# Kernel tuning notes

Hardware: AMD Instinct MI355X
Metric: run time of the kernel (lower is better)

Reference implementation:

```python
import jax, jax.numpy as jnp
import numpy as np

K = 20          # knn neighbors (includes self, as in DGL KNNGraph)
EPS = 1e-5      # BatchNorm eps
SLOPE = 0.2     # leaky relu slope


def knn_idx(h, k):
    # h: [B,N,D]; k smallest pairwise squared distances (self included)
    d2 = jnp.sum(h * h, axis=-1)                                # [B,N]
    dist = d2[:, :, None] + d2[:, None, :] - 2.0 * jnp.einsum('bnd,bmd->bnm', h, h)
    _, idx = jax.lax.top_k(-dist, k)                            # [B,N,k] neighbor indices
    return idx


def edge_conv(h, idx, Wt, bt, Wp, bp, gamma, beta):
    # DGL EdgeConv with batch_norm=True (training-mode batch stats):
    # edges: src=neighbor j, dst=point i;  m_ij = theta(x_i - x_j) + phi(x_j)
    xj = jax.vmap(lambda hb, ib: hb[ib])(h, idx)                # [B,N,k,D] gathered neighbors
    m = (jnp.einsum('bnkd,do->bnko', h[:, :, None, :] - xj, Wt) + bt
         + jnp.einsum('bnkd,do->bnko', xj, Wp) + bp)            # [B,N,k,O]
    mu = jnp.mean(m, axis=(0, 1, 2))
    var = jnp.var(m, axis=(0, 1, 2))
    m = (m - mu) * jax.lax.rsqrt(var + EPS) * gamma + beta
    return jnp.max(m, axis=2)                                   # max aggregate over neighbors


def setup_inputs() -> dict:
    key = jax.random.key(0)
    ks = jax.random.split(key, 20)
    s = 0.05
    d_in, d0, d1, d_feat, d_out = 3, 64, 256, 512, 256
    return {
        'x':   jax.random.normal(ks[0], (4, 4096, d_in), jnp.float32),
        'Wt0': jax.random.normal(ks[1], (d_in, d0), jnp.float32) * s,
        'bt0': jnp.zeros((d0,), jnp.float32),
        'Wp0': jax.random.normal(ks[2], (d_in, d0), jnp.float32) * s,
        'bp0': jnp.zeros((d0,), jnp.float32),
        'g0':  jnp.ones((d0,), jnp.float32),
        'be0': jnp.zeros((d0,), jnp.float32),
        'Wt1': jax.random.normal(ks[3], (d0, d1), jnp.float32) * s,
        'bt1': jnp.zeros((d1,), jnp.float32),
        'Wp1': jax.random.normal(ks[4], (d0, d1), jnp.float32) * s,
        'bp1': jnp.zeros((d1,), jnp.float32),
        'g1':  jnp.ones((d1,), jnp.float32),
        'be1': jnp.zeros((d1,), jnp.float32),
        'Wg':  jax.random.normal(ks[5], (d1, 1), jnp.float32) * s,
        'bg':  jnp.zeros((1,), jnp.float32),
        'Wf':  jax.random.normal(ks[6], (d1, d_feat), jnp.float32) * s,
        'bf':  jnp.zeros((d_feat,), jnp.float32),
        'Wl':  jax.random.normal(ks[7], (d_feat, d_out), jnp.float32) * s,
        'bl':  jnp.zeros((d_out,), jnp.float32),
    }


def reference(x, Wt0, bt0, Wp0, bp0, g0, be0,
              Wt1, bt1, Wp1, bp1, g1, be1,
              Wg, bg, Wf, bf, Wl, bl):
    # layer 0: knn on raw points, EdgeConv 3->64, leaky relu
    h = x
    idx = knn_idx(h, K)
    h = jax.nn.leaky_relu(edge_conv(h, idx, Wt0, bt0, Wp0, bp0, g0, be0), SLOPE)
    # layer 1: knn on 64-d features, EdgeConv 64->256, leaky relu
    idx = knn_idx(h, K)
    h = jax.nn.leaky_relu(edge_conv(h, idx, Wt1, bt1, Wp1, bp1, g1, be1), SLOPE)
    # global attention pooling (softmax over nodes within each cloud)
    gate = jax.nn.relu(h @ Wg + bg)                 # [B,N,1]
    feat = jax.nn.relu(h @ Wf + bf)                 # [B,N,512]
    alpha = jax.nn.softmax(gate, axis=1)
    pooled = jnp.sum(alpha * feat, axis=1)          # [B,512]
    return pooled @ Wl + bl                         # [B,256]
```

## Files before the change

kernel.cpp:

```cpp
#include <hip/hip_runtime.h>
#include <hip/hip_bf16.h>
#include <math.h>

static constexpr int NBATCH = 4;
static constexpr int NPTS   = 4096;
static constexpr int BN     = NBATCH * NPTS;
static constexpr int KNN    = 20;
static constexpr float BN_EPS = 1e-5f;
static constexpr float SLOPE  = 0.2f;
static constexpr int DF = 512, DOUT = 256;

#define FINF __builtin_huge_valf()

typedef short bf16x8 __attribute__((ext_vector_type(8)));
typedef float f32x4  __attribute__((ext_vector_type(4)));

static constexpr size_t OFF_H0     = 0;
static constexpr size_t OFF_IDX0   = 4194304;
static constexpr size_t OFF_IDX1   = 5505024;
static constexpr size_t OFF_D2     = 6815744;
static constexpr size_t OFF_GATE   = 6881280;
static constexpr size_t OFF_ALPHA  = 6946816;
static constexpr size_t OFF_SS0    = 7012352;
static constexpr size_t OFF_SS1    = 7012864;
static constexpr size_t OFF_STATS0 = 7014912;
static constexpr size_t OFF_STATS1 = 7015424;
static constexpr size_t OFF_POOLED = 7017472;
static constexpr size_t ZERO_OFF   = OFF_STATS0;
static constexpr size_t ZERO_BYTES = 7025664 - 7014912;
static constexpr size_t OFF_P1     = 7025664;
static constexpr size_t OFF_PDU    = OFF_P1;
static constexpr size_t OFF_WQK    = 23802880;
static constexpr size_t OFF_WFK    = 23933952;
static constexpr size_t OFF_Q1     = 27997184;
static constexpr size_t OFF_U0     = OFF_Q1;
static constexpr size_t OFF_V0     = OFF_Q1 + 1048576;
static constexpr size_t OFF_P0     = OFF_Q1;
static constexpr size_t OFF_Q0     = OFF_Q1 + 2097152;
static constexpr size_t OFF_H1     = 44774400;
static constexpr size_t OFF_AB     = 61551616;

__device__ inline unsigned short f2bf_rne(float x) {
  unsigned int u = __float_as_uint(x);
  unsigned int lsb = (u >> 16) & 1u;
  u += 0x7fffu + lsb;
  return (unsigned short)(u >> 16);
}
__device__ inline float bf2f(unsigned short s) {
  return __uint_as_float((unsigned int)s << 16);
}
__device__ inline unsigned umn(unsigned a, unsigned b) { return a < b ? a : b; }
__device__ inline unsigned umed3(unsigned v, unsigned lo, unsigned hi) {
  unsigned d;
  asm("v_med3_u32 %0, %1, %2, %3" : "=v"(d) : "v"(v), "v"(lo), "v"(hi));
  return d;
}

__global__ __launch_bounds__(256) void d2x_kernel(const float* __restrict__ x,
                                                  float* __restrict__ d2) {
  int n = blockIdx.x * 256 + threadIdx.x;
  const float* r = x + (size_t)n * 3;
  d2[n] = r[0] * r[0] + r[1] * r[1] + r[2] * r[2];
}

__global__ __launch_bounds__(256) void usplit0_kernel(
    const float* __restrict__ x, unsigned short* __restrict__ U0,
    unsigned short* __restrict__ V0) {
  int n = blockIdx.x * 256 + threadIdx.x;
  float v0 = x[(size_t)n * 3], v1 = x[(size_t)n * 3 + 1], v2 = x[(size_t)n * 3 + 2];
  unsigned short A0 = f2bf_rne(v0), A1 = f2bf_rne(v1), A2 = f2bf_rne(v2);
  unsigned short B0 = f2bf_rne(v0 - bf2f(A0));
  unsigned short B1 = f2bf_rne(v1 - bf2f(A1));
  unsigned short B2 = f2bf_rne(v2 - bf2f(A2));
  ushort4 z = make_ushort4(0, 0, 0, 0);
  unsigned short* up = U0 + ((size_t)n << 5);
  ((ushort4*)up)[0] = make_ushort4(A0, A1, A2, B0);
  ((ushort4*)up)[1] = make_ushort4(B1, B2, A0, A1);
  ((ushort4*)up)[2] = make_ushort4(A2, B0, B1, B2);
  ((ushort4*)up)[3] = z; ((ushort4*)up)[4] = z; ((ushort4*)up)[5] = z;
  ((ushort4*)up)[6] = z; ((ushort4*)up)[7] = z;
  unsigned short* vp = V0 + ((size_t)n << 5);
  ((ushort4*)vp)[0] = make_ushort4(A0, A1, A2, A0);
  ((ushort4*)vp)[1] = make_ushort4(A1, A2, B0, B1);
  ((ushort4*)vp)[2] = make_ushort4(B2, B0, B1, B2);
  ((ushort4*)vp)[3] = z; ((ushort4*)vp)[4] = z; ((ushort4*)vp)[5] = z;
  ((ushort4*)vp)[6] = z; ((ushort4*)vp)[7] = z;
}

template<int KW, int CST, int S>
__global__ __launch_bounds__(256, 4) void knn_mfsel_kernel(
    const unsigned short* __restrict__ cab,
    const unsigned short* __restrict__ qab,
    const float* __restrict__ d2,
    unsigned* __restrict__ pdu) {
  constexpr int CS = NPTS / S, NCH = CS / 32;
  __shared__ __align__(16) unsigned short cbuf[2][32 * CST];
  __shared__ __align__(16) float cd2b[2][32];

  int bid = blockIdx.x;
  int s   = bid & (S - 1);
  int qb  = bid / S;
  int b   = qb >> 6;
  int qloc = (qb & 63) * 64;
  int wv = threadIdx.x >> 6, lane = threadIdx.x & 63;
  int l15 = lane & 15, lg = lane >> 4;
  int qg = b * NPTS + qloc + wv * 16 + l15;

  bf16x8 af[KW / 32];
#pragma unroll
  for (int kk = 0; kk < KW / 32; ++kk)
    af[kk] = *(const bf16x8*)(qab + (size_t)qg * KW + kk * 32 + lg * 8);
  float d2q = d2[qg];

  unsigned bd[KNN];
#pragma unroll
  for (int k = 0; k < KNN; ++k) bd[k] = 0xFFFFFFFFu;

  int scand = threadIdx.x >> 3, sseg = threadIdx.x & 7;
  const unsigned short* sbase = cab + ((size_t)(b * NPTS + s * CS)) * KW;
  const float* d2base = d2 + b * NPTS + s * CS;

  bf16x8 r0, r1;
  ushort4 r2;
  float rd2 = 0.f;

  if constexpr (KW == 128) {
    const unsigned short* src = sbase + (size_t)scand * KW + sseg * 16;
    r0 = *(const bf16x8*)src;
    r1 = *(const bf16x8*)(src + 8);
    *(bf16x8*)&cbuf[0][scand * CST + sseg * 16]     = r0;
    *(bf16x8*)&cbuf[0][scand * CST + sseg * 16 + 8] = r1;
  } else {
    r2 = *(const ushort4*)(sbase + (size_t)scand * KW + sseg * 4);
    *(ushort4*)&cbuf[0][scand * CST + sseg * 4] = r2;
  }
  if (threadIdx.x < 32) cd2b[0][threadIdx.x] = d2base[threadIdx.x];
  __syncthreads();

#pragma unroll 1
  for (int ch = 0; ch < NCH; ++ch) {
    int cur = ch & 1;
    if (ch < NCH - 1) {
      if constexpr (KW == 128) {
        const unsigned short* src = sbase + (size_t)(32 * (ch + 1) + scand) * KW + sseg * 16;
        r0 = *(const bf16x8*)src;
        r1 = *(const bf16x8*)(src + 8);
      } else {
        r2 = *(const ushort4*)(sbase + (size_t)(32 * (ch + 1) + scand) * KW + sseg * 4);
      }
      if (threadIdx.x < 32) rd2 = d2base[32 * (ch + 1) + threadIdx.x];
    }

    f32x4 acc0 = (f32x4){0.f, 0.f, 0.f, 0.f};
    f32x4 acc1 = (f32x4){0.f, 0.f, 0.f, 0.f};
    if constexpr (KW == 128) {
#pragma unroll
      for (int j = 0; j < 4; ++j) {
        int koff = j * 32 + lg * 8;
        bf16x8 a0 = *(const bf16x8*)&cbuf[cur][l15 * CST + koff];
        bf16x8 a1 = *(const bf16x8*)&cbuf[cur][(16 + l15) * CST + koff];
        acc0 = __builtin_amdgcn_mfma_f32_16x16x32_bf16(a0, af[j], acc0, 0, 0, 0);
        acc0 = __builtin_amdgcn_mfma_f32_16x16x32_bf16(a0, af[(j + 2) & 3], acc0, 0, 0, 0);
        acc1 = __builtin_amdgcn_mfma_f32_16x16x32_bf16(a1, af[j], acc1, 0, 0, 0);
        acc1 = __builtin_amdgcn_mfma_f32_16x16x32_bf16(a1, af[(j + 2) & 3], acc1, 0, 0, 0);
      }
    } else {
      bf16x8 a0 = *(const bf16x8*)&cbuf[cur][l15 * CST + lg * 8];
      bf16x8 a1 = *(const bf16x8*)&cbuf[cur][(16 + l15) * CST + lg * 8];
      acc0 = __builtin_amdgcn_mfma_f32_16x16x32_bf16(a0, af[0], acc0, 0, 0, 0);
      acc1 = __builtin_amdgcn_mfma_f32_16x16x32_bf16(a1, af[0], acc1, 0, 0, 0);
    }

    int cb = s * CS + ch * 32;
#pragma unroll
    for (int t = 0; t < 2; ++t) {
      f32x4 cd4 = *(const f32x4*)&cd2b[cur][t * 16 + lg * 4];
      f32x4 ac = t ? acc1 : acc0;
#pragma unroll
      for (int r = 0; r < 4; ++r) {
        float dist = fmaxf(fmaf(-2.f, ac[r], d2q + cd4[r]), 0.f);
        unsigned key = (__float_as_uint(dist) & 0xFFFFF000u)
                     | (unsigned)(cb + t * 16 + lg * 4 + r);
#pragma unroll
        for (int t_ = KNN - 1; t_ >= 1; --t_) bd[t_] = umed3(key, bd[t_ - 1], bd[t_]);
        bd[0] = umn(bd[0], key);
      }
    }

    if (ch < NCH - 1) {
      if constexpr (KW == 128) {
        *(bf16x8*)&cbuf[cur ^ 1][scand * CST + sseg * 16]     = r0;
        *(bf16x8*)&cbuf[cur ^ 1][scand * CST + sseg * 16 + 8] = r1;
      } else {
        *(ushort4*)&cbuf[cur ^ 1][scand * CST + sseg * 4] = r2;
      }
      if (threadIdx.x < 32) cd2b[cur ^ 1][threadIdx.x] = rd2;
    }
    __syncthreads();
  }

#pragma unroll 1
  for (int li = 1; li < 4; ++li) {
#pragma unroll 1
    for (int k = 0; k < KNN; ++k) {
      unsigned v = __shfl(bd[k], l15 + li * 16, 64);
      if (lg == 0 && v < bd[KNN - 1]) {
#pragma unroll
        for (int t_ = KNN - 1; t_ >= 1; --t_) bd[t_] = umed3(v, bd[t_ - 1], bd[t_]);
        bd[0] = umn(bd[0], v);
      }
    }
  }
  if (lg == 0) {
    unsigned* dst = pdu + ((size_t)(b * NPTS + qloc + wv * 16 + l15) * S + s) * KNN;
#pragma unroll
    for (int k = 0; k < KNN; ++k) dst[k] = bd[k];
  }
}

template<int S>
__global__ __launch_bounds__(256) void knn_mergek_kernel(
    const unsigned* __restrict__ pdu, int* __restrict__ idx) {
  int n = blockIdx.x * 256 + threadIdx.x;
  const unsigned* l0 = pdu + (size_t)n * S * KNN;
  unsigned bd[KNN];
#pragma unroll
  for (int k = 0; k < KNN; ++k) bd[k] = l0[k];
#pragma unroll 1
  for (int s = 1; s < S; ++s) {
#pragma unroll 1
    for (int k = 0; k < KNN; ++k) {
      unsigned v = l0[s * KNN + k];
      if (!(v < bd[KNN - 1])) break;
#pragma unroll
      for (int t_ = KNN - 1; t_ >= 1; --t_) bd[t_] = umed3(v, bd[t_ - 1], bd[t_]);
      bd[0] = umn(bd[0], v);
    }
  }
#pragma unroll
  for (int k = 0; k < KNN; ++k) idx[(size_t)n * KNN + k] = (int)(bd[k] & 0xFFFu);
}

__global__ __launch_bounds__(256) void pq0_kernel(
    const float* __restrict__ x,
    const float* __restrict__ Wt, const float* __restrict__ bt,
    const float* __restrict__ Wp, const float* __restrict__ bp,
    unsigned short* __restrict__ P0, unsigned short* __restrict__ Q0) {
  int t = blockIdx.x * 256 + threadIdx.x;
  int c = t & 63, n = t >> 6;
  const float* xr = x + (size_t)n * 3;
  float x0 = xr[0], x1 = xr[1], x2 = xr[2];
  float wt0 = Wt[0 * 64 + c], wt1 = Wt[1 * 64 + c], wt2 = Wt[2 * 64 + c];
  float wp0 = Wp[0 * 64 + c], wp1 = Wp[1 * 64 + c], wp2 = Wp[2 * 64 + c];
  P0[t] = f2bf_rne(x0 * wt0 + x1 * wt1 + x2 * wt2 + bt[c] + bp[c]);
  Q0[t] = f2bf_rne(x0 * (wp0 - wt0) + x1 * (wp1 - wt1) + x2 * (wp2 - wt2));
}

template<int C, int PB>
__global__ __launch_bounds__(256) void bn_gather_kernel(
    const unsigned short* __restrict__ P, const unsigned short* __restrict__ Q,
    const int* __restrict__ idx, float* __restrict__ stats,
    unsigned* __restrict__ vmm) {
  constexpr int G = 256 / C;
  int c = threadIdx.x % C;
  int g = threadIdx.x / C;
  int p0 = blockIdx.x * PB;
  float sum = 0.f, sq = 0.f;
  for (int p = g; p < PB; p += G) {
    int n = p0 + p;
    int b = n >> 12;
    float pc = bf2f(P[(size_t)n * C + c]);
    const int* id = idx + (size_t)n * KNN;
    float vmax = -FINF, vmin = FINF;
#pragma unroll
    for (int k = 0; k < KNN; ++k) {
      int j = id[k];
      float v = pc + bf2f(Q[((size_t)(b << 12) + j) * C + c]);
      sum += v; sq += v * v;
      vmax = fmaxf(vmax, v); vmin = fminf(vmin, v);
    }
    vmm[(size_t)n * C + c] = ((unsigned)f2bf_rne(vmax) << 16) | f2bf_rne(vmin);
  }
  if constexpr (G > 1) {
    __shared__ float ls[2][256];
    ls[0][threadIdx.x] = sum; ls[1][threadIdx.x] = sq;
    __syncthreads();
    if (g == 0) {
#pragma unroll
      for (int gg = 1; gg < G; ++gg) { sum += ls[0][gg * C + c]; sq += ls[1][gg * C + c]; }
      atomicAdd(&stats[c], sum); atomicAdd(&stats[C + c], sq);
    }
  } else {
    atomicAdd(&stats[c], sum); atomicAdd(&stats[C + c], sq);
  }
}

template<int C>
__global__ void bn_final_kernel(const float* __restrict__ stats,
                                const float* __restrict__ gamma,
                                const float* __restrict__ beta,
                                float* __restrict__ ss) {
  int c = threadIdx.x;
  if (c < C) {
    const float cnt = (float)((size_t)BN * KNN);
    float mu  = stats[c] / cnt;
    float var = stats[C + c] / cnt - mu * mu;
    float sc  = gamma[c] * rsqrtf(var + BN_EPS);
    ss[c] = sc;
    ss[C + c] = beta[c] - mu * sc;
  }
}

__global__ __launch_bounds__(256) void apply0_kernel(
    const unsigned* __restrict__ vmm, const float* __restrict__ ss,
    unsigned short* __restrict__ ab, float* __restrict__ d2) {
  int wv = threadIdx.x >> 6, lane = threadIdx.x & 63;
  int n = blockIdx.x * 4 + wv;
  unsigned pk = vmm[(size_t)n * 64 + lane];
  float sc = ss[lane], sh = ss[64 + lane];
  float vmax = bf2f((unsigned short)(pk >> 16));
  float vmin = bf2f((unsigned short)(pk & 0xFFFFu));
  float m = (sc >= 0.f) ? vmax : vmin;
  float y = fmaf(m, sc, sh);
  y = (y >= 0.f) ? y : SLOPE * y;
  unsigned short a = f2bf_rne(y);
  unsigned short b = f2bf_rne(y - bf2f(a));
  ab[(size_t)n * 128 + lane] = a;
  ab[(size_t)n * 128 + 64 + lane] = b;
  float s = y * y;
#pragma unroll
  for (int off = 32; off >= 1; off >>= 1) s += __shfl_down(s, off);
  if (lane == 0) d2[n] = s;
}

__global__ __launch_bounds__(256) void wprep1_kernel(
    const float* __restrict__ Wt, const float* __restrict__ Wp,
    unsigned short* __restrict__ wqk) {
  int t = blockIdx.x * 256 + threadIdx.x;
  int o = t >> 6, k = t & 63;
  float w;
  if (o < 256) w = Wt[(size_t)k * 256 + o];
  else { int oo = o - 256; w = Wp[(size_t)k * 256 + oo] - Wt[(size_t)k * 256 + oo]; }
  unsigned short a = f2bf_rne(w);
  wqk[(size_t)o * 128 + k]      = a;
  wqk[(size_t)o * 128 + 64 + k] = f2bf_rne(w - bf2f(a));
}

__global__ __launch_bounds__(256) void wprepf_kernel(
    const float* __restrict__ Wf, unsigned short* __restrict__ wfk) {
  int t = blockIdx.x * 256 + threadIdx.x;
  int o = t >> 8, k = t & 255;
  float w = Wf[(size_t)k * 512 + o];
  unsigned short a = f2bf_rne(w);
  wfk[(size_t)o * 512 + k]       = a;
  wfk[(size_t)o * 512 + 256 + k] = f2bf_rne(w - bf2f(a));
}

__global__ __launch_bounds__(256, 2) void gemm_pq1_kernel(
    const unsigned short* __restrict__ ab, const unsigned short* __restrict__ wqk,
    const float* __restrict__ bt, const float* __restrict__ bp,
    unsigned short* __restrict__ P1, unsigned short* __restrict__ Q1) {
  __shared__ __align__(16) unsigned short As[64 * 136];
  int cb = blockIdx.x & 1;
  int rb = blockIdx.x >> 1;
  int wv = threadIdx.x >> 6, lane = threadIdx.x & 63;
  int l15 = lane & 15, lg = lane >> 4;
  {
    int row = threadIdx.x >> 2, seg = threadIdx.x & 3;
    const unsigned short* src = ab + ((size_t)(rb * 64 + row)) * 128 + seg * 32;
    *(bf16x8*)&As[row * 136 + seg * 32]      = *(const bf16x8*)(src);
    *(bf16x8*)&As[row * 136 + seg * 32 + 8]  = *(const bf16x8*)(src + 8);
    *(bf16x8*)&As[row * 136 + seg * 32 + 16] = *(const bf16x8*)(src + 16);
    *(bf16x8*)&As[row * 136 + seg * 32 + 24] = *(const bf16x8*)(src + 24);
  }
  __syncthreads();
  int wcol = cb * 256 + wv * 64;
  f32x4 acc[4][4];
#pragma unroll
  for (int m = 0; m < 4; ++m)
#pragma unroll
    for (int n = 0; n < 4; ++n) acc[m][n] = (f32x4){0.f, 0.f, 0.f, 0.f};
#pragma unroll
  for (int kk = 0; kk < 4; ++kk) {
    int k0 = kk * 32 + lg * 8;
    int k1 = ((kk + 2) & 3) * 32 + lg * 8;
    bf16x8 am[4], b0[4], b1[4];
#pragma unroll
    for (int m = 0; m < 4; ++m)
      am[m] = *(const bf16x8*)&As[(m * 16 + l15) * 136 + k0];
#pragma unroll
    for (int n = 0; n < 4; ++n) {
      const unsigned short* wr = wqk + (size_t)(wcol + n * 16 + l15) * 128;
      b0[n] = *(const bf16x8*)(wr + k0);
      b1[n] = *(const bf16x8*)(wr + k1);
    }
#pragma unroll
    for (int m = 0; m < 4; ++m)
#pragma unroll
      for (int n = 0; n < 4; ++n) {
        acc[m][n] = __builtin_amdgcn_mfma_f32_16x16x32_bf16(am[m], b0[n], acc[m][n], 0, 0, 0);
        acc[m][n] = __builtin_amdgcn_mfma_f32_16x16x32_bf16(am[m], b1[n], acc[m][n], 0, 0, 0);
      }
  }
#pragma unroll
  for (int n = 0; n < 4; ++n) {
    int col = wcol + n * 16 + l15;
    bool isP = col < 256;
    float bias = isP ? (bt[col] + bp[col]) : 0.f;
    unsigned short* dst = isP ? (P1 + col) : (Q1 + (col - 256));
#pragma unroll
    for (int m = 0; m < 4; ++m)
#pragma unroll
      for (int r = 0; r < 4; ++r) {
        int row = rb * 64 + m * 16 + lg * 4 + r;
        dst[(size_t)row * 256] = f2bf_rne(acc[m][n][r] + bias);
      }
  }
}

__global__ __launch_bounds__(256) void apply1_kernel(
    const unsigned* __restrict__ vmm, const float* __restrict__ ss,
    const float* __restrict__ Wg, const float* __restrict__ bg,
    unsigned short* __restrict__ ab1, float* __restrict__ gate) {
  int wv = threadIdx.x >> 6, lane = threadIdx.x & 63;
  int n = blockIdx.x * 4 + wv;
  unsigned pk[4];
#pragma unroll
  for (int i = 0; i < 4; ++i) pk[i] = vmm[(size_t)n * 256 + lane + 64 * i];
  float gsum = 0.f;
  unsigned short Aa[4], Bb[4];
#pragma unroll
  for (int i = 0; i < 4; ++i) {
    int c = lane + 64 * i;
    float sc = ss[c], sh = ss[256 + c];
    float vmax = bf2f((unsigned short)(pk[i] >> 16));
    float vmin = bf2f((unsigned short)(pk[i] & 0xFFFFu));
    float m = (sc >= 0.f) ? vmax : vmin;
    float y = fmaf(m, sc, sh);
    y = (y >= 0.f) ? y : SLOPE * y;
    Aa[i] = f2bf_rne(y);
    Bb[i] = f2bf_rne(y - bf2f(Aa[i]));
    gsum += y * Wg[c];
  }
#pragma unroll
  for (int i = 0; i < 4; ++i) {
    ab1[(size_t)n * 512 + lane + 64 * i]       = Aa[i];
    ab1[(size_t)n * 512 + 256 + lane + 64 * i] = Bb[i];
  }
#pragma unroll
  for (int off = 32; off >= 1; off >>= 1) gsum += __shfl_down(gsum, off);
  if (lane == 0) gate[n] = fmaxf(gsum + bg[0], 0.f);
}

__global__ void softmax_kernel(const float* __restrict__ gate,
                               float* __restrict__ alpha) {
  __shared__ float red[256];
  int b = blockIdx.x;
  const float* g = gate + (size_t)b * NPTS;
  float* a = alpha + (size_t)b * NPTS;
  float m = -FINF;
  for (int i = threadIdx.x; i < NPTS; i += 256) m = fmaxf(m, g[i]);
  red[threadIdx.x] = m; __syncthreads();
  for (int st = 128; st >= 1; st >>= 1) {
    if (threadIdx.x < st) red[threadIdx.x] = fmaxf(red[threadIdx.x], red[threadIdx.x + st]);
    __syncthreads();
  }
  m = red[0]; __syncthreads();
  float s = 0.f;
  for (int i = threadIdx.x; i < NPTS; i += 256) s += expf(g[i] - m);
  red[threadIdx.x] = s; __syncthreads();
  for (int st = 128; st >= 1; st >>= 1) {
    if (threadIdx.x < st) red[threadIdx.x] += red[threadIdx.x + st];
    __syncthreads();
  }
  float inv = 1.f / red[0];
  for (int i = threadIdx.x; i < NPTS; i += 256) a[i] = expf(g[i] - m) * inv;
}

__global__ __launch_bounds__(256, 2) void gemm_fp_kernel(
    const unsigned short* __restrict__ ab1, const unsigned short* __restrict__ wfk,
    const float* __restrict__ bf, const float* __restrict__ alpha,
    float* __restrict__ pooled) {
  __shared__ __align__(16) unsigned short As[2][64 * 136];
  int cb = blockIdx.x & 1;
  int rb = blockIdx.x >> 1;
  int wv = threadIdx.x >> 6, lane = threadIdx.x & 63;
  int l15 = lane & 15, lg = lane >> 4;
  int wcol = cb * 256 + wv * 64;
  int rowbase = rb * 64;
  f32x4 acc[4][4];
#pragma unroll
  for (int m = 0; m < 4; ++m)
#pragma unroll
    for (int n = 0; n < 4; ++n) acc[m][n] = (f32x4){0.f, 0.f, 0.f, 0.f};

#pragma unroll 1
  for (int kc = 0; kc < 2; ++kc) {
    __syncthreads();
    {
      int row = threadIdx.x >> 2, seg = threadIdx.x & 3;
      const unsigned short* s0 = ab1 + ((size_t)(rowbase + row)) * 512 + kc * 128 + seg * 32;
      const unsigned short* s1 = s0 + 256;
#pragma unroll
      for (int u = 0; u < 4; ++u) {
        *(bf16x8*)&As[0][row * 136 + seg * 32 + u * 8] = *(const bf16x8*)(s0 + u * 8);
        *(bf16x8*)&As[1][row * 136 + seg * 32 + u * 8] = *(const bf16x8*)(s1 + u * 8);
      }
    }
    __syncthreads();
#pragma unroll
    for (int h = 0; h < 2; ++h) {
#pragma unroll
      for (int kk = 0; kk < 4; ++kk) {
        int s  = kc * 4 + h * 8 + kk;
        int sp = (s + 8) & 15;
        int lk = kk * 32 + lg * 8;
        bf16x8 am[4], b0[4], b1[4];
#pragma unroll
        for (int m = 0; m < 4; ++m)
          am[m] = *(const bf16x8*)&As[h][(m * 16 + l15) * 136 + lk];
#pragma unroll
        for (int n = 0; n < 4; ++n) {
          const unsigned short* wr = wfk + (size_t)(wcol + n * 16 + l15) * 512;
          b0[n] = *(const bf16x8*)(wr + s * 32 + lg * 8);
          b1[n] = *(const bf16x8*)(wr + sp * 32 + lg * 8);
        }
#pragma unroll
        for (int m = 0; m < 4; ++m)
#pragma unroll
          for (int n = 0; n < 4; ++n) {
            acc[m][n] = __builtin_amdgcn_mfma_f32_16x16x32_bf16(am[m], b0[n], acc[m][n], 0, 0, 0);
            acc[m][n] = __builtin_amdgcn_mfma_f32_16x16x32_bf16(am[m], b1[n], acc[m][n], 0, 0, 0);
          }
      }
    }
  }
  int b = rowbase >> 12;
  float al[4][4];
#pragma unroll
  for (int m = 0; m < 4; ++m)
#pragma unroll
    for (int r = 0; r < 4; ++r)
      al[m][r] = alpha[rowbase + m * 16 + lg * 4 + r];
#pragma unroll
  for (int n = 0; n < 4; ++n) {
    int col = wcol + n * 16 + l15;
    float bv = bf[col];
    float po = 0.f;
#pragma unroll
    for (int m = 0; m < 4; ++m)
#pragma unroll
      for (int r = 0; r < 4; ++r)
        po += al[m][r] * fmaxf(acc[m][n][r] + bv, 0.f);
    po += __shfl_xor(po, 16, 64);
    po += __shfl_xor(po, 32, 64);
    if (lg == 0) atomicAdd(&pooled[(size_t)b * DF + col], po);
  }
}

__global__ __launch_bounds__(256) void final_kernel(
    const float* __restrict__ pooled, const float* __restrict__ Wl,
    const float* __restrict__ bl, float* __restrict__ out) {
  __shared__ float ps[DF];
  int b = blockIdx.x, j = threadIdx.x;
  for (int e = threadIdx.x; e < DF; e += 256) ps[e] = pooled[(size_t)b * DF + e];
  __syncthreads();
  float a0 = 0.f, a1 = 0.f, a2 = 0.f, a3 = 0.f;
  for (int o = 0; o < DF; o += 4) {
    a0 += ps[o + 0] * Wl[(size_t)(o + 0) * DOUT + j];
    a1 += ps[o + 1] * Wl[(size_t)(o + 1) * DOUT + j];
    a2 += ps[o + 2] * Wl[(size_t)(o + 2) * DOUT + j];
    a3 += ps[o + 3] * Wl[(size_t)(o + 3) * DOUT + j];
  }
  out[(size_t)b * DOUT + j] = (a0 + a1) + (a2 + a3) + bl[j];
}

extern "C" void kernel_launch(void* const* d_in, const int* in_sizes, int n_in,
                              void* d_out, int out_size, void* d_ws, size_t ws_size,
                              hipStream_t stream) {
  (void)in_sizes; (void)n_in; (void)out_size; (void)ws_size;
  const float* x   = (const float*)d_in[0];
  const float* Wt0 = (const float*)d_in[1];
  const float* bt0 = (const float*)d_in[2];
  const float* Wp0 = (const float*)d_in[3];
  const float* bp0 = (const float*)d_in[4];
  const float* g0  = (const float*)d_in[5];
  const float* be0 = (const float*)d_in[6];
  const float* Wt1 = (const float*)d_in[7];
  const float* bt1 = (const float*)d_in[8];
  const float* Wp1 = (const float*)d_in[9];
  const float* bp1 = (const float*)d_in[10];
  const float* g1  = (const float*)d_in[11];
  const float* be1 = (const float*)d_in[12];
  const float* Wg  = (const float*)d_in[13];
  const float* bg  = (const float*)d_in[14];
  const float* Wf  = (const float*)d_in[15];
  const float* bf  = (const float*)d_in[16];
  const float* Wl  = (const float*)d_in[17];
  const float* bl  = (const float*)d_in[18];
  float* out = (float*)d_out;
  char* ws = (char*)d_ws;

  unsigned* VMM0 = (unsigned*)(ws + OFF_H0);
  int*   IDX0   = (int*)  (ws + OFF_IDX0);
  int*   IDX1   = (int*)  (ws + OFF_IDX1);
  float* D2     = (float*)(ws + OFF_D2);
  float* GATE   = (float*)(ws + OFF_GATE);
  float* ALPHA  = (float*)(ws + OFF_ALPHA);
  float* SS0    = (float*)(ws + OFF_SS0);
  float* SS1    = (float*)(ws + OFF_SS1);
  float* STATS0 = (float*)(ws + OFF_STATS0);
  float* STATS1 = (float*)(ws + OFF_STATS1);
  float* POOLED = (float*)(ws + OFF_POOLED);
  unsigned short* P1 = (unsigned short*)(ws + OFF_P1);
  unsigned short* Q1 = (unsigned short*)(ws + OFF_Q1);
  unsigned* VMM1 = (unsigned*)(ws + OFF_H1);
  unsigned short* AB1 = (unsigned short*)(ws + OFF_H1);
  unsigned short* P0 = (unsigned short*)(ws + OFF_P0);
  unsigned short* Q0 = (unsigned short*)(ws + OFF_Q0);
  unsigned short* AB = (unsigned short*)(ws + OFF_AB);
  unsigned* PDU = (unsigned*)(ws + OFF_PDU);
  unsigned short* U0 = (unsigned short*)(ws + OFF_U0);
  unsigned short* V0 = (unsigned short*)(ws + OFF_V0);
  unsigned short* WQK = (unsigned short*)(ws + OFF_WQK);
  unsigned short* WFK = (unsigned short*)(ws + OFF_WFK);

  hipMemsetAsync(ws + ZERO_OFF, 0, ZERO_BYTES, stream);

  wprep1_kernel<<<512 * 64 / 256, 256, 0, stream>>>(Wt1, Wp1, WQK);
  wprepf_kernel<<<512 * 256 / 256, 256, 0, stream>>>(Wf, WFK);

  d2x_kernel<<<BN / 256, 256, 0, stream>>>(x, D2);
  usplit0_kernel<<<BN / 256, 256, 0, stream>>>(x, U0, V0);
  knn_mfsel_kernel<32, 40, 4><<<(BN / 64) * 4, 256, 0, stream>>>(V0, U0, D2, PDU);
  knn_mergek_kernel<4><<<BN / 256, 256, 0, stream>>>(PDU, IDX0);
  pq0_kernel<<<BN * 64 / 256, 256, 0, stream>>>(x, Wt0, bt0, Wp0, bp0, P0, Q0);
  bn_gather_kernel<64, 32><<<BN / 32, 256, 0, stream>>>(P0, Q0, IDX0, STATS0, VMM0);
  bn_final_kernel<64><<<1, 64, 0, stream>>>(STATS0, g0, be0, SS0);
  apply0_kernel<<<BN / 4, 256, 0, stream>>>(VMM0, SS0, AB, D2);

  knn_mfsel_kernel<128, 136, 4><<<(BN / 64) * 4, 256, 0, stream>>>(AB, AB, D2, PDU);
  knn_mergek_kernel<4><<<BN / 256, 256, 0, stream>>>(PDU, IDX1);
  gemm_pq1_kernel<<<(BN / 64) * 2, 256, 0, stream>>>(AB, WQK, bt1, bp1, P1, Q1);
  bn_gather_kernel<256, 16><<<BN / 16, 256, 0, stream>>>(P1, Q1, IDX1, STATS1, VMM1);
  bn_final_kernel<256><<<1, 256, 0, stream>>>(STATS1, g1, be1, SS1);
  apply1_kernel<<<BN / 4, 256, 0, stream>>>(VMM1, SS1, Wg, bg, AB1, GATE);

  softmax_kernel<<<NBATCH, 256, 0, stream>>>(GATE, ALPHA);
  gemm_fp_kernel<<<(BN / 64) * 2, 256, 0, stream>>>(AB1, WFK, bf, ALPHA, POOLED);
  final_kernel<<<NBATCH, 256, 0, stream>>>(POOLED, Wl, bl, out);
}
```

Measured before the change: 417.2 us.

## Swizzle LDS tiles, reorder weight layout, and fuse small prep/BN-final kernels

```diff
diff --git a/kernel.cpp b/kernel.cpp
--- a/kernel.cpp
+++ b/kernel.cpp
@@ -21,8 +21,6 @@
 static constexpr size_t OFF_D2     = 6815744;
 static constexpr size_t OFF_GATE   = 6881280;
 static constexpr size_t OFF_ALPHA  = 6946816;
-static constexpr size_t OFF_SS0    = 7012352;
-static constexpr size_t OFF_SS1    = 7012864;
 static constexpr size_t OFF_STATS0 = 7014912;
 static constexpr size_t OFF_STATS1 = 7015424;
 static constexpr size_t OFF_POOLED = 7017472;
@@ -56,18 +54,12 @@
   return d;
 }
 
-__global__ __launch_bounds__(256) void d2x_kernel(const float* __restrict__ x,
-                                                  float* __restrict__ d2) {
-  int n = blockIdx.x * 256 + threadIdx.x;
-  const float* r = x + (size_t)n * 3;
-  d2[n] = r[0] * r[0] + r[1] * r[1] + r[2] * r[2];
-}
-
-__global__ __launch_bounds__(256) void usplit0_kernel(
-    const float* __restrict__ x, unsigned short* __restrict__ U0,
-    unsigned short* __restrict__ V0) {
+__global__ __launch_bounds__(256) void prep0_kernel(
+    const float* __restrict__ x, float* __restrict__ d2,
+    unsigned short* __restrict__ U0, unsigned short* __restrict__ V0) {
   int n = blockIdx.x * 256 + threadIdx.x;
   float v0 = x[(size_t)n * 3], v1 = x[(size_t)n * 3 + 1], v2 = x[(size_t)n * 3 + 2];
+  d2[n] = v0 * v0 + v1 * v1 + v2 * v2;
   unsigned short A0 = f2bf_rne(v0), A1 = f2bf_rne(v1), A2 = f2bf_rne(v2);
   unsigned short B0 = f2bf_rne(v0 - bf2f(A0));
   unsigned short B1 = f2bf_rne(v1 - bf2f(A1));
@@ -87,6 +79,32 @@
   ((ushort4*)vp)[6] = z; ((ushort4*)vp)[7] = z;
 }
 
+__global__ __launch_bounds__(256) void wprep_kernel(
+    const float* __restrict__ Wt, const float* __restrict__ Wp,
+    const float* __restrict__ Wf,
+    unsigned short* __restrict__ wqk, unsigned short* __restrict__ wfk) {
+  int bid = blockIdx.x;
+  if (bid < 128) {
+    int t = bid * 256 + threadIdx.x;
+    int o = t >> 6, k = t & 63;
+    float w;
+    if (o < 256) w = Wt[(size_t)k * 256 + o];
+    else { int oo = o - 256; w = Wp[(size_t)k * 256 + oo] - Wt[(size_t)k * 256 + oo]; }
+    unsigned short a = f2bf_rne(w);
+    unsigned short b = f2bf_rne(w - bf2f(a));
+    wqk[((size_t)(k >> 3) * 512 + o) * 8 + (k & 7)]          = a;
+    wqk[((size_t)((k + 64) >> 3) * 512 + o) * 8 + (k & 7)]   = b;
+  } else {
+    int t = (bid - 128) * 256 + threadIdx.x;
+    int o = t >> 8, k = t & 255;
+    float w = Wf[(size_t)k * 512 + o];
+    unsigned short a = f2bf_rne(w);
+    unsigned short b = f2bf_rne(w - bf2f(a));
+    wfk[((size_t)(k >> 3) * 512 + o) * 8 + (k & 7)]          = a;
+    wfk[((size_t)((k + 256) >> 3) * 512 + o) * 8 + (k & 7)]  = b;
+  }
+}
+
 template<int KW, int CST, int S>
 __global__ __launch_bounds__(256, 4) void knn_mfsel_kernel(
     const unsigned short* __restrict__ cab,
@@ -128,8 +146,9 @@
     const unsigned short* src = sbase + (size_t)scand * KW + sseg * 16;
     r0 = *(const bf16x8*)src;
     r1 = *(const bf16x8*)(src + 8);
-    *(bf16x8*)&cbuf[0][scand * CST + sseg * 16]     = r0;
-    *(bf16x8*)&cbuf[0][scand * CST + sseg * 16 + 8] = r1;
+    int s0 = (2 * sseg) ^ (scand & 7), s1 = (2 * sseg + 1) ^ (scand & 7);
+    *(bf16x8*)&cbuf[0][scand * 128 + s0 * 8] = r0;
+    *(bf16x8*)&cbuf[0][scand * 128 + s1 * 8] = r1;
   } else {
     r2 = *(const ushort4*)(sbase + (size_t)scand * KW + sseg * 4);
     *(ushort4*)&cbuf[0][scand * CST + sseg * 4] = r2;
@@ -156,9 +175,9 @@
     if constexpr (KW == 128) {
 #pragma unroll
       for (int j = 0; j < 4; ++j) {
-        int koff = j * 32 + lg * 8;
-        bf16x8 a0 = *(const bf16x8*)&cbuf[cur][l15 * CST + koff];
-        bf16x8 a1 = *(const bf16x8*)&cbuf[cur][(16 + l15) * CST + koff];
+        int blk = (4 * j + lg) ^ (l15 & 7);
+        bf16x8 a0 = *(const bf16x8*)&cbuf[cur][l15 * 128 + blk * 8];
+        bf16x8 a1 = *(const bf16x8*)&cbuf[cur][(16 + l15) * 128 + blk * 8];
         acc0 = __builtin_amdgcn_mfma_f32_16x16x32_bf16(a0, af[j], acc0, 0, 0, 0);
         acc0 = __builtin_amdgcn_mfma_f32_16x16x32_bf16(a0, af[(j + 2) & 3], acc0, 0, 0, 0);
         acc1 = __builtin_amdgcn_mfma_f32_16x16x32_bf16(a1, af[j], acc1, 0, 0, 0);
@@ -189,8 +208,9 @@
 
     if (ch < NCH - 1) {
       if constexpr (KW == 128) {
-        *(bf16x8*)&cbuf[cur ^ 1][scand * CST + sseg * 16]     = r0;
-        *(bf16x8*)&cbuf[cur ^ 1][scand * CST + sseg * 16 + 8] = r1;
+        int s0 = (2 * sseg) ^ (scand & 7), s1 = (2 * sseg + 1) ^ (scand & 7);
+        *(bf16x8*)&cbuf[cur ^ 1][scand * 128 + s0 * 8] = r0;
+        *(bf16x8*)&cbuf[cur ^ 1][scand * 128 + s1 * 8] = r1;
       } else {
         *(ushort4*)&cbuf[cur ^ 1][scand * CST + sseg * 4] = r2;
       }
@@ -295,29 +315,25 @@
   }
 }
 
-template<int C>
-__global__ void bn_final_kernel(const float* __restrict__ stats,
-                                const float* __restrict__ gamma,
-                                const float* __restrict__ beta,
-                                float* __restrict__ ss) {
-  int c = threadIdx.x;
-  if (c < C) {
+__global__ __launch_bounds__(256) void apply0_kernel(
+    const unsigned* __restrict__ vmm, const float* __restrict__ stats,
+    const float* __restrict__ gamma, const float* __restrict__ beta,
+    unsigned short* __restrict__ ab, float* __restrict__ d2) {
+  __shared__ float ssl[128];
+  if (threadIdx.x < 64) {
+    int c = threadIdx.x;
     const float cnt = (float)((size_t)BN * KNN);
     float mu  = stats[c] / cnt;
-    float var = stats[C + c] / cnt - mu * mu;
+    float var = stats[64 + c] / cnt - mu * mu;
     float sc  = gamma[c] * rsqrtf(var + BN_EPS);
-    ss[c] = sc;
-    ss[C + c] = beta[c] - mu * sc;
-  }
-}
-
-__global__ __launch_bounds__(256) void apply0_kernel(
-    const unsigned* __restrict__ vmm, const float* __restrict__ ss,
-    unsigned short* __restrict__ ab, float* __restrict__ d2) {
+    ssl[c] = sc;
+    ssl[64 + c] = beta[c] - mu * sc;
+  }
+  __syncthreads();
   int wv = threadIdx.x >> 6, lane = threadIdx.x & 63;
   int n = blockIdx.x * 4 + wv;
   unsigned pk = vmm[(size_t)n * 64 + lane];
-  float sc = ss[lane], sh = ss[64 + lane];
+  float sc = ssl[lane], sh = ssl[64 + lane];
   float vmax = bf2f((unsigned short)(pk >> 16));
   float vmin = bf2f((unsigned short)(pk & 0xFFFFu));
   float m = (sc >= 0.f) ? vmax : vmin;
@@ -333,34 +349,11 @@
   if (lane == 0) d2[n] = s;
 }
 
-__global__ __launch_bounds__(256) void wprep1_kernel(
-    const float* __restrict__ Wt, const float* __restrict__ Wp,
-    unsigned short* __restrict__ wqk) {
-  int t = blockIdx.x * 256 + threadIdx.x;
-  int o = t >> 6, k = t & 63;
-  float w;
-  if (o < 256) w = Wt[(size_t)k * 256 + o];
-  else { int oo = o - 256; w = Wp[(size_t)k * 256 + oo] - Wt[(size_t)k * 256 + oo]; }
-  unsigned short a = f2bf_rne(w);
-  wqk[(size_t)o * 128 + k]      = a;
-  wqk[(size_t)o * 128 + 64 + k] = f2bf_rne(w - bf2f(a));
-}
-
-__global__ __launch_bounds__(256) void wprepf_kernel(
-    const float* __restrict__ Wf, unsigned short* __restrict__ wfk) {
-  int t = blockIdx.x * 256 + threadIdx.x;
-  int o = t >> 8, k = t & 255;
-  float w = Wf[(size_t)k * 512 + o];
-  unsigned short a = f2bf_rne(w);
-  wfk[(size_t)o * 512 + k]       = a;
-  wfk[(size_t)o * 512 + 256 + k] = f2bf_rne(w - bf2f(a));
-}
-
 __global__ __launch_bounds__(256, 2) void gemm_pq1_kernel(
     const unsigned short* __restrict__ ab, const unsigned short* __restrict__ wqk,
     const float* __restrict__ bt, const float* __restrict__ bp,
     unsigned short* __restrict__ P1, unsigned short* __restrict__ Q1) {
-  __shared__ __align__(16) unsigned short As[64 * 136];
+  __shared__ __align__(16) unsigned short As[64 * 128];
   int cb = blockIdx.x & 1;
   int rb = blockIdx.x >> 1;
   int wv = threadIdx.x >> 6, lane = threadIdx.x & 63;
@@ -368,10 +361,11 @@
   {
     int row = threadIdx.x >> 2, seg = threadIdx.x & 3;
     const unsigned short* src = ab + ((size_t)(rb * 64 + row)) * 128 + seg * 32;
-    *(bf16x8*)&As[row * 136 + seg * 32]      = *(const bf16x8*)(src);
-    *(bf16x8*)&As[row * 136 + seg * 32 + 8]  = *(const bf16x8*)(src + 8);
-    *(bf16x8*)&As[row * 136 + seg * 32 + 16] = *(const bf16x8*)(src + 16);
-    *(bf16x8*)&As[row * 136 + seg * 32 + 24] = *(const bf16x8*)(src + 24);
+#pragma unroll
+    for (int u = 0; u < 4; ++u) {
+      int blk = (seg * 4 + u) ^ (row & 7);
+      *(bf16x8*)&As[row * 128 + blk * 8] = *(const bf16x8*)(src + u * 8);
+    }
   }
   __syncthreads();
   int wcol = cb * 256 + wv * 64;
@@ -382,17 +376,19 @@
     for (int n = 0; n < 4; ++n) acc[m][n] = (f32x4){0.f, 0.f, 0.f, 0.f};
 #pragma unroll
   for (int kk = 0; kk < 4; ++kk) {
-    int k0 = kk * 32 + lg * 8;
-    int k1 = ((kk + 2) & 3) * 32 + lg * 8;
+    int k8a = kk * 4 + lg;
+    int k8b = ((kk + 2) & 3) * 4 + lg;
     bf16x8 am[4], b0[4], b1[4];
 #pragma unroll
-    for (int m = 0; m < 4; ++m)
-      am[m] = *(const bf16x8*)&As[(m * 16 + l15) * 136 + k0];
+    for (int m = 0; m < 4; ++m) {
+      int row = m * 16 + l15;
+      am[m] = *(const bf16x8*)&As[row * 128 + (k8a ^ (l15 & 7)) * 8];
+    }
 #pragma unroll
     for (int n = 0; n < 4; ++n) {
-      const unsigned short* wr = wqk + (size_t)(wcol + n * 16 + l15) * 128;
-      b0[n] = *(const bf16x8*)(wr + k0);
-      b1[n] = *(const bf16x8*)(wr + k1);
+      int col = wcol + n * 16 + l15;
+      b0[n] = *(const bf16x8*)(wqk + ((size_t)k8a * 512 + col) * 8);
+      b1[n] = *(const bf16x8*)(wqk + ((size_t)k8b * 512 + col) * 8);
     }
 #pragma unroll
     for (int m = 0; m < 4; ++m)
@@ -419,9 +415,21 @@
 }
 
 __global__ __launch_bounds__(256) void apply1_kernel(
-    const unsigned* __restrict__ vmm, const float* __restrict__ ss,
+    const unsigned* __restrict__ vmm, const float* __restrict__ stats,
+    const float* __restrict__ gamma, const float* __restrict__ beta,
     const float* __restrict__ Wg, const float* __restrict__ bg,
     unsigned short* __restrict__ ab1, float* __restrict__ gate) {
+  __shared__ float ssl[512];
+  {
+    int c = threadIdx.x;
+    const float cnt = (float)((size_t)BN * KNN);
+    float mu  = stats[c] / cnt;
+    float var = stats[256 + c] / cnt - mu * mu;
+    float sc  = gamma[c] * rsqrtf(var + BN_EPS);
+    ssl[c] = sc;
+    ssl[256 + c] = beta[c] - mu * sc;
+  }
+  __syncthreads();
   int wv = threadIdx.x >> 6, lane = threadIdx.x & 63;
   int n = blockIdx.x * 4 + wv;
   unsigned pk[4];
@@ -432,7 +440,7 @@
 #pragma unroll
   for (int i = 0; i < 4; ++i) {
     int c = lane + 64 * i;
-    float sc = ss[c], sh = ss[256 + c];
+    float sc = ssl[c], sh = ssl[256 + c];
     float vmax = bf2f((unsigned short)(pk[i] >> 16));
     float vmin = bf2f((unsigned short)(pk[i] & 0xFFFFu));
     float m = (sc >= 0.f) ? vmax : vmin;
@@ -481,7 +489,7 @@
     const unsigned short* __restrict__ ab1, const unsigned short* __restrict__ wfk,
     const float* __restrict__ bf, const float* __restrict__ alpha,
     float* __restrict__ pooled) {
-  __shared__ __align__(16) unsigned short As[2][64 * 136];
+  __shared__ __align__(16) unsigned short As[2][64 * 128];
   int cb = blockIdx.x & 1;
   int rb = blockIdx.x >> 1;
   int wv = threadIdx.x >> 6, lane = threadIdx.x & 63;
@@ -503,8 +511,9 @@
       const unsigned short* s1 = s0 + 256;
 #pragma unroll
       for (int u = 0; u < 4; ++u) {
-        *(bf16x8*)&As[0][row * 136 + seg * 32 + u * 8] = *(const bf16x8*)(s0 + u * 8);
-        *(bf16x8*)&As[1][row * 136 + seg * 32 + u * 8] = *(const bf16x8*)(s1 + u * 8);
+        int blk = (seg * 4 + u) ^ (row & 7);
+        *(bf16x8*)&As[0][row * 128 + blk * 8] = *(const bf16x8*)(s0 + u * 8);
+        *(bf16x8*)&As[1][row * 128 + blk * 8] = *(const bf16x8*)(s1 + u * 8);
       }
     }
     __syncthreads();
@@ -514,16 +523,17 @@
       for (int kk = 0; kk < 4; ++kk) {
         int s  = kc * 4 + h * 8 + kk;
         int sp = (s + 8) & 15;
-        int lk = kk * 32 + lg * 8;
         bf16x8 am[4], b0[4], b1[4];
 #pragma unroll
-        for (int m = 0; m < 4; ++m)
-          am[m] = *(const bf16x8*)&As[h][(m * 16 + l15) * 136 + lk];
+        for (int m = 0; m < 4; ++m) {
+          int row = m * 16 + l15;
+          am[m] = *(const bf16x8*)&As[h][row * 128 + ((kk * 4 + lg) ^ (l15 & 7)) * 8];
+        }
 #pragma unroll
         for (int n = 0; n < 4; ++n) {
-          const unsigned short* wr = wfk + (size_t)(wcol + n * 16 + l15) * 512;
-          b0[n] = *(const bf16x8*)(wr + s * 32 + lg * 8);
-          b1[n] = *(const bf16x8*)(wr + sp * 32 + lg * 8);
+          int col = wcol + n * 16 + l15;
+          b0[n] = *(const bf16x8*)(wfk + ((size_t)(s * 4 + lg) * 512 + col) * 8);
+          b1[n] = *(const bf16x8*)(wfk + ((size_t)(sp * 4 + lg) * 512 + col) * 8);
         }
 #pragma unroll
         for (int m = 0; m < 4; ++m)
@@ -607,8 +617,6 @@
   float* D2     = (float*)(ws + OFF_D2);
   float* GATE   = (float*)(ws + OFF_GATE);
   float* ALPHA  = (float*)(ws + OFF_ALPHA);
-  float* SS0    = (float*)(ws + OFF_SS0);
-  float* SS1    = (float*)(ws + OFF_SS1);
   float* STATS0 = (float*)(ws + OFF_STATS0);
   float* STATS1 = (float*)(ws + OFF_STATS1);
   float* POOLED = (float*)(ws + OFF_POOLED);
@@ -627,24 +635,20 @@
 
   hipMemsetAsync(ws + ZERO_OFF, 0, ZERO_BYTES, stream);
 
-  wprep1_kernel<<<512 * 64 / 256, 256, 0, stream>>>(Wt1, Wp1, WQK);
-  wprepf_kernel<<<512 * 256 / 256, 256, 0, stream>>>(Wf, WFK);
-
-  d2x_kernel<<<BN / 256, 256, 0, stream>>>(x, D2);
-  usplit0_kernel<<<BN / 256, 256, 0, stream>>>(x, U0, V0);
+  wprep_kernel<<<128 + 512, 256, 0, stream>>>(Wt1, Wp1, Wf, WQK, WFK);
+
+  prep0_kernel<<<BN / 256, 256, 0, stream>>>(x, D2, U0, V0);
   knn_mfsel_kernel<32, 40, 4><<<(BN / 64) * 4, 256, 0, stream>>>(V0, U0, D2, PDU);
   knn_mergek_kernel<4><<<BN / 256, 256, 0, stream>>>(PDU, IDX0);
   pq0_kernel<<<BN * 64 / 256, 256, 0, stream>>>(x, Wt0, bt0, Wp0, bp0, P0, Q0);
   bn_gather_kernel<64, 32><<<BN / 32, 256, 0, stream>>>(P0, Q0, IDX0, STATS0, VMM0);
-  bn_final_kernel<64><<<1, 64, 0, stream>>>(STATS0, g0, be0, SS0);
-  apply0_kernel<<<BN / 4, 256, 0, stream>>>(VMM0, SS0, AB, D2);
-
-  knn_mfsel_kernel<128, 136, 4><<<(BN / 64) * 4, 256, 0, stream>>>(AB, AB, D2, PDU);
+  apply0_kernel<<<BN / 4, 256, 0, stream>>>(VMM0, STATS0, g0, be0, AB, D2);
+
+  knn_mfsel_kernel<128, 128, 4><<<(BN / 64) * 4, 256, 0, stream>>>(AB, AB, D2, PDU);
   knn_mergek_kernel<4><<<BN / 256, 256, 0, stream>>>(PDU, IDX1);
   gemm_pq1_kernel<<<(BN / 64) * 2, 256, 0, stream>>>(AB, WQK, bt1, bp1, P1, Q1);
   bn_gather_kernel<256, 16><<<BN / 16, 256, 0, stream>>>(P1, Q1, IDX1, STATS1, VMM1);
-  bn_final_kernel<256><<<1, 256, 0, stream>>>(STATS1, g1, be1, SS1);
-  apply1_kernel<<<BN / 4, 256, 0, stream>>>(VMM1, SS1, Wg, bg, AB1, GATE);
+  apply1_kernel<<<BN / 4, 256, 0, stream>>>(VMM1, STATS1, g1, be1, Wg, bg, AB1, GATE);
 
   softmax_kernel<<<NBATCH, 256, 0, stream>>>(GATE, ALPHA);
   gemm_fp_kernel<<<(BN / 64) * 2, 256, 0, stream>>>(AB1, WFK, bf, ALPHA, POOLED);
```

New measurement: 410.5 us. No clear change (-1.6%).
